# Optimization experiments

Measured on AMD Instinct MI355X. Metric: run time of the kernel, lower is better.

Reference implementation:

```python
import jax, jax.numpy as jnp
import numpy as np

B, M_IN, N_OUT = 131072, 64, 64


def setup_inputs() -> dict:
    key = jax.random.key(0)
    k1, k2, k3 = jax.random.split(key, 3)
    x = jax.random.normal(k1, (B, M_IN, 4), dtype=jnp.float32)
    x = x.at[:, :, 0].set(0.0)  # pure quaternion input (w-component = 0)
    stdv_w = (2.0 / (M_IN + N_OUT)) ** 0.5
    W_q = jax.random.normal(k2, (N_OUT, M_IN, 4), dtype=jnp.float32) * (stdv_w / 2.0)
    theta_q = jax.random.normal(k3, (N_OUT, 4), dtype=jnp.float32) * 0.01
    theta_q = theta_q.at[:, 0].set(0.0)  # pure quaternion threshold
    return {"x_batch": x, "W_q": W_q, "theta_q": theta_q}


def _hamilton_sum(x, W):
    """s[b,n] = sum_m W[n,m] (x) x[b,m]  (Hamilton product, W on the left).
    x: (B, M, 4), W: (N, M, 4) -> (B, N, 4)"""
    ww, wx, wy, wz = (W[..., i] for i in range(4))   # each (N, M)
    xw, xx, xy, xz = (x[..., i] for i in range(4))   # each (B, M)
    dot = lambda p, q: jnp.einsum('bm,nm->bn', p, q)
    sw = dot(xw, ww) - dot(xx, wx) - dot(xy, wy) - dot(xz, wz)
    sx = dot(xx, ww) + dot(xw, wx) + dot(xz, wy) - dot(xy, wz)
    sy = dot(xy, ww) - dot(xz, wx) + dot(xw, wy) + dot(xx, wz)
    sz = dot(xz, ww) + dot(xy, wx) - dot(xx, wy) + dot(xw, wz)
    return jnp.stack([sw, sx, sy, sz], axis=-1)


def reference(x_batch, W_q, theta_q):
    # Isokawa quaternion neuron: s = sum_m W (x) x - theta; y = sigmoid(s) per component.
    s = _hamilton_sum(x_batch, W_q) - theta_q[None, :, :]  # (B, N, 4) pre-activation (s_internal)
    return jax.nn.sigmoid(s)
```

## Files before the change

### kernel.cpp

```cpp
#include <hip/hip_runtime.h>
#include <hip/hip_bf16.h>


typedef __bf16 bf16_t;
typedef bf16_t bf16x8 __attribute__((ext_vector_type(8)));
typedef bf16_t bf16x4v __attribute__((ext_vector_type(4)));
typedef float f32x4 __attribute__((ext_vector_type(4)));

#define B_TOTAL 131072
#define KDIM 256
#define NDIM 256
#define ROWS 64
#define THREADS 512
#define LDS_STRIDE 264
#define TPB 4
#define GRID (B_TOTAL / (ROWS * TPB))

__global__ void coef_kernel(const float* __restrict__ W, bf16_t* __restrict__ coef) {
    const int widx[4][4] = {{0,1,2,3},{1,0,3,2},{2,3,0,1},{3,2,1,0}};
    const float sgn[4][4] = {{1.f,-1.f,-1.f,-1.f},
                             {1.f, 1.f,-1.f, 1.f},
                             {1.f, 1.f, 1.f,-1.f},
                             {1.f,-1.f, 1.f, 1.f}};
    int F = blockIdx.x * blockDim.x + threadIdx.x;
    int j    = F & 7;
    int lane = (F >> 3) & 63;
    int ks   = (F >> 9) & 7;
    int nt   = F >> 12;
    int col  = nt * 16 + (lane & 15);
    int k    = ks * 32 + (lane >> 4) * 8 + j;
    int n = col >> 2, oc = col & 3;
    int m = k >> 2,   ic = k & 3;
    coef[F] = (bf16_t)(sgn[oc][ic] * W[n * 256 + m * 4 + widx[oc][ic]]);
}

__global__ __launch_bounds__(THREADS, 2)
void main_kernel(const float* __restrict__ x, const bf16x8* __restrict__ coef,
                 const float* __restrict__ theta, float* __restrict__ out) {
    __shared__ __align__(16) bf16_t xs[ROWS * LDS_STRIDE];

    const int tid  = threadIdx.x;
    const int wave = tid >> 6, lane = tid & 63;
    const int l15  = lane & 15, quad = lane >> 4;
    const long tile0 = (long)blockIdx.x * TPB;
    const float4* xbase = (const float4*)x;

    float4 v[8];
    {
        const float4* xp = xbase + tile0 * (ROWS * KDIM / 4);
#pragma unroll
        for (int i = 0; i < 8; i++) v[i] = xp[tid + THREADS * i];
    }

    bf16x8 breg[2][8];
#pragma unroll
    for (int ct = 0; ct < 2; ct++)
#pragma unroll
        for (int ks = 0; ks < 8; ks++)
            breg[ct][ks] = coef[((wave * 2 + ct) * 8 + ks) * 64 + lane];

    f32x4 th4[2];
#pragma unroll
    for (int ct = 0; ct < 2; ct++)
        th4[ct] = *(const f32x4*)&theta[wave * 32 + ct * 16 + quad * 4];

#pragma unroll
    for (int t = 0; t < TPB; t++) {
        const float4* xq = xbase + (tile0 + t + 1) * (ROWS * KDIM / 4);
#pragma unroll
        for (int i = 0; i < 8; i++) {
            int f = tid + THREADS * i;
            int r = f >> 6;
            int c = (f & 63) * 4;
            bf16x4v w;
            w.x = (bf16_t)v[i].x; w.y = (bf16_t)v[i].y;
            w.z = (bf16_t)v[i].z; w.w = (bf16_t)v[i].w;
            *(bf16x4v*)&xs[r * LDS_STRIDE + c] = w;
            if (t + 1 < TPB) v[i] = xq[tid + THREADS * i];
        }

        asm volatile("s_waitcnt lgkmcnt(0)" ::: "memory");
        __builtin_amdgcn_s_barrier();

        f32x4 acc[4][2];
#pragma unroll
        for (int rt = 0; rt < 4; rt++)
#pragma unroll
            for (int ct = 0; ct < 2; ct++) acc[rt][ct] = (f32x4)(0.f);

#pragma unroll
        for (int ks = 0; ks < 8; ks++) {
            bf16x8 a[4];
#pragma unroll
            for (int rt = 0; rt < 4; rt++)
                a[rt] = *(const bf16x8*)&xs[(rt * 16 + l15) * LDS_STRIDE + ks * 32 + quad * 8];
#pragma unroll
            for (int rt = 0; rt < 4; rt++)
#pragma unroll
                for (int ct = 0; ct < 2; ct++)
                    acc[rt][ct] = __builtin_amdgcn_mfma_f32_16x16x32_bf16(
                        breg[ct][ks], a[rt], acc[rt][ct], 0, 0, 0);
        }

        asm volatile("s_waitcnt lgkmcnt(0)" ::: "memory");
        __builtin_amdgcn_s_barrier();

        const long row0 = (tile0 + t) * ROWS;
#pragma unroll
        for (int rt = 0; rt < 4; rt++) {
            long row = row0 + rt * 16 + l15;
#pragma unroll
            for (int ct = 0; ct < 2; ct++) {
                f32x4 y;
#pragma unroll
                for (int j = 0; j < 4; j++) {
                    float s = acc[rt][ct][j] - th4[ct][j];
                    y[j] = __builtin_amdgcn_rcpf(1.0f + __expf(-s));
                }
                *(f32x4*)&out[row * NDIM + wave * 32 + ct * 16 + quad * 4] = y;
            }
        }
    }
}

extern "C" void kernel_launch(void* const* d_in, const int* in_sizes, int n_in,
                              void* d_out, int out_size, void* d_ws, size_t ws_size,
                              hipStream_t stream) {
    const float* x     = (const float*)d_in[0];
    const float* W     = (const float*)d_in[1];
    const float* theta = (const float*)d_in[2];
    float* out = (float*)d_out;
    bf16_t* coef = (bf16_t*)d_ws;

    if (ws_size < 65536 * sizeof(bf16_t)) return;

    coef_kernel<<<256, 256, 0, stream>>>(W, coef);
    main_kernel<<<GRID, THREADS, 0, stream>>>(
        x, (const bf16x8*)coef, theta, out);
}
```

Baseline: 247.1 us.

## Stream fp32 x tiles into double-buffered LDS via async global_load_lds

Replaces the register-staged load, bf16 convert and LDS store of x with direct global-to-LDS async copies of raw fp32 into two swizzled LDS buffers. Tiles per block double to 8, and vmcnt waits track a two-tile prefetch depth. The fp32-to-bf16 conversion moves to the read side, so every wave converts the same A fragments redundantly. The 128KB LDS footprint limits the kernel to one block per CU, so it relies on the async overlap to hide memory latency instead of a second resident block.

```diff
diff --git a/kernel.cpp b/kernel.cpp
--- a/kernel.cpp
+++ b/kernel.cpp
@@ -4,7 +4,6 @@
 
 typedef __bf16 bf16_t;
 typedef bf16_t bf16x8 __attribute__((ext_vector_type(8)));
-typedef bf16_t bf16x4v __attribute__((ext_vector_type(4)));
 typedef float f32x4 __attribute__((ext_vector_type(4)));
 
 #define B_TOTAL 131072
@@ -12,8 +11,7 @@
 #define NDIM 256
 #define ROWS 64
 #define THREADS 512
-#define LDS_STRIDE 264
-#define TPB 4
+#define TPB 8
 #define GRID (B_TOTAL / (ROWS * TPB))
 
 __global__ void coef_kernel(const float* __restrict__ W, bf16_t* __restrict__ coef) {
@@ -37,20 +35,12 @@
 __global__ __launch_bounds__(THREADS, 2)
 void main_kernel(const float* __restrict__ x, const bf16x8* __restrict__ coef,
                  const float* __restrict__ theta, float* __restrict__ out) {
-    __shared__ __align__(16) bf16_t xs[ROWS * LDS_STRIDE];
+    __shared__ __align__(16) float xs[2][ROWS * KDIM];
 
     const int tid  = threadIdx.x;
     const int wave = tid >> 6, lane = tid & 63;
     const int l15  = lane & 15, quad = lane >> 4;
     const long tile0 = (long)blockIdx.x * TPB;
-    const float4* xbase = (const float4*)x;
-
-    float4 v[8];
-    {
-        const float4* xp = xbase + tile0 * (ROWS * KDIM / 4);
-#pragma unroll
-        for (int i = 0; i < 8; i++) v[i] = xp[tid + THREADS * i];
-    }
 
     bf16x8 breg[2][8];
 #pragma unroll
@@ -64,23 +54,38 @@
     for (int ct = 0; ct < 2; ct++)
         th4[ct] = *(const f32x4*)&theta[wave * 32 + ct * 16 + quad * 4];
 
-#pragma unroll
-    for (int t = 0; t < TPB; t++) {
-        const float4* xq = xbase + (tile0 + t + 1) * (ROWS * KDIM / 4);
+    auto stage = [&](int t) {
+        const float* src = x + (tile0 + t) * (long)(ROWS * KDIM);
+        float* dst = &xs[t & 1][0];
 #pragma unroll
         for (int i = 0; i < 8; i++) {
-            int f = tid + THREADS * i;
-            int r = f >> 6;
-            int c = (f & 63) * 4;
-            bf16x4v w;
-            w.x = (bf16_t)v[i].x; w.y = (bf16_t)v[i].y;
-            w.z = (bf16_t)v[i].z; w.w = (bf16_t)v[i].w;
-            *(bf16x4v*)&xs[r * LDS_STRIDE + c] = w;
-            if (t + 1 < TPB) v[i] = xq[tid + THREADS * i];
+            int s   = i * THREADS + tid;
+            int row = s >> 6;
+            int c16 = (s & 63) ^ (row & 7);
+            __builtin_amdgcn_global_load_lds(
+                (const __attribute__((address_space(1))) void*)(src + row * KDIM + c16 * 4),
+                (__attribute__((address_space(3))) void*)(dst + (long)s * 4),
+                16, 0, 0);
         }
+    };
 
-        asm volatile("s_waitcnt lgkmcnt(0)" ::: "memory");
+    stage(0);
+    stage(1);
+
+    const int sw = l15 & 7;
+    int rowoff[4];
+#pragma unroll
+    for (int rt = 0; rt < 4; rt++) rowoff[rt] = (rt * 16 + l15) * KDIM;
+
+#pragma unroll 1
+    for (int t = 0; t < TPB; t++) {
+        if (t == 0 || t == TPB - 1)
+            asm volatile("s_waitcnt vmcnt(8)" ::: "memory");
+        else
+            asm volatile("s_waitcnt vmcnt(16)" ::: "memory");
         __builtin_amdgcn_s_barrier();
+
+        const float* buf = &xs[t & 1][0];
 
         f32x4 acc[4][2];
 #pragma unroll
@@ -92,8 +97,18 @@
         for (int ks = 0; ks < 8; ks++) {
             bf16x8 a[4];
 #pragma unroll
-            for (int rt = 0; rt < 4; rt++)
-                a[rt] = *(const bf16x8*)&xs[(rt * 16 + l15) * LDS_STRIDE + ks * 32 + quad * 8];
+            for (int rt = 0; rt < 4; rt++) {
+                int cA = ((ks * 8 + quad * 2)     ^ sw) * 4;
+                int cB = ((ks * 8 + quad * 2 + 1) ^ sw) * 4;
+                f32x4 lo = *(const f32x4*)&buf[rowoff[rt] + cA];
+                f32x4 hi = *(const f32x4*)&buf[rowoff[rt] + cB];
+                bf16x8 af;
+                af[0] = (bf16_t)lo[0]; af[1] = (bf16_t)lo[1];
+                af[2] = (bf16_t)lo[2]; af[3] = (bf16_t)lo[3];
+                af[4] = (bf16_t)hi[0]; af[5] = (bf16_t)hi[1];
+                af[6] = (bf16_t)hi[2]; af[7] = (bf16_t)hi[3];
+                a[rt] = af;
+            }
 #pragma unroll
             for (int rt = 0; rt < 4; rt++)
 #pragma unroll
@@ -120,6 +135,9 @@
                 *(f32x4*)&out[row * NDIM + wave * 32 + ct * 16 + quad * 4] = y;
             }
         }
+
+        asm volatile("" ::: "memory");
+        if (t + 2 < TPB) stage(t + 2);
     }
 }
 
```

Result: no change. 249.1 us (+0.8%).
